# Kernel tuning notes

Hardware: AMD Instinct MI355X
Metric: run time of the kernel (lower is better)

## Reference

```python
import jax, jax.numpy as jnp
import numpy as np


def setup_inputs() -> dict:
    key = jax.random.key(0)
    inputs = jax.random.normal(key, (8, 4096, 512), dtype=jnp.float32)
    return {"inputs": inputs}


def reference(inputs) -> jnp.ndarray:
    # Faithful math: out = (X @ X^T) @ X  per batch.
    # Expressed via the associativity-equivalent X @ (X^T @ X), which computes
    # the identical result while avoiding the O(S^2) intermediate (S >> D).
    gram = jnp.einsum('bsd,bse->bde', inputs, inputs)   # [B, D, D]
    out = jnp.einsum('bsd,bde->bse', inputs, gram)      # [B, S, D]
    return out
```

## Files before the change

### kernel.cpp

```cpp
#include <hip/hip_runtime.h>
#include <hip/hip_bf16.h>


typedef __attribute__((ext_vector_type(8))) short short8;
typedef __attribute__((ext_vector_type(4))) float floatx4;

#define BM 128
#define BN 128
#define BK 32

#define BATCH 8
#define SEQ 4096
#define DIM 512
#define NSPLIT_K2 4

__device__ __forceinline__ void async_copy16(const __hip_bfloat16* g, __hip_bfloat16* l) {
  __builtin_amdgcn_global_load_lds((const __attribute__((address_space(1))) void*)g,
                                   (__attribute__((address_space(3))) void*)l, 16, 0, 0);
}

__global__ __launch_bounds__(256) void transpose_cast_kernel(
    const float* __restrict__ X, __hip_bfloat16* __restrict__ Xt) {
  __shared__ float tile[64][65];
  const int b = blockIdx.z;
  const int s0 = blockIdx.x * 64;
  const int d0 = blockIdx.y * 64;
  const int tid = threadIdx.x;
  const int tx = tid & 63;
  const int ty = tid >> 6;
  const float* Xb = X + (long)b * SEQ * DIM;
  __hip_bfloat16* Xtb = Xt + (long)b * DIM * SEQ;
#pragma unroll
  for (int r = 0; r < 64; r += 4)
    tile[r + ty][tx] = Xb[(long)(s0 + r + ty) * DIM + d0 + tx];
  __syncthreads();
#pragma unroll
  for (int it = 0; it < 2; ++it) {
    const int idx = it * 256 + tid;
    const int dl = idx >> 3;
    const int so = (idx & 7) * 8;
    union { short8 v; __hip_bfloat16 e[8]; } u;
#pragma unroll
    for (int j = 0; j < 8; ++j) u.e[j] = __float2bfloat16(tile[so + j][dl]);
    *(short8*)&Xtb[(long)(d0 + dl) * SEQ + s0 + so] = u.v;
  }
}

template <int NSPLIT, bool AFP32>
__global__ __launch_bounds__(256) void gemm_bt_kernel(
    const float* __restrict__ Af, const __hip_bfloat16* __restrict__ Ab,
    const __hip_bfloat16* __restrict__ Bt, float* __restrict__ C,
    int K, int lda, int ldb, int ldc, long strideA, long strideB, long strideC) {
  __shared__ __align__(16) __hip_bfloat16 As[BM * BK];
  __shared__ __align__(16) __hip_bfloat16 Bs[BN * BK];

  const int bz = blockIdx.z;
  const int b = bz / NSPLIT;
  const int split = bz % NSPLIT;
  const int klen = K / NSPLIT;
  const int kb = split * klen;

  const int m0 = blockIdx.y * BM;
  const int n0 = blockIdx.x * BN;
  const int tid = threadIdx.x;
  const int w = tid >> 6;
  const int lane = tid & 63;
  const int r16 = lane & 15;
  const int kg = lane >> 4;
  const int wr = w >> 1;
  const int wc = w & 1;

  const float* Afb = AFP32 ? Af + b * strideA : nullptr;
  const __hip_bfloat16* Abb = AFP32 ? nullptr : Ab + b * strideA;
  const __hip_bfloat16* Btb = Bt + b * strideB;
  float* Cb = C + (long)bz * strideC;

  const floatx4 vzero = {0.f, 0.f, 0.f, 0.f};
  floatx4 acc[4][4];
#pragma unroll
  for (int i = 0; i < 4; ++i)
#pragma unroll
    for (int j = 0; j < 4; ++j) acc[i][j] = vzero;

  for (int k0 = kb; k0 < kb + klen; k0 += BK) {
#pragma unroll
    for (int q = 0; q < 2; ++q) {
      const __hip_bfloat16* gb =
          Btb + (long)(n0 + w * 32 + q * 16 + (lane >> 2)) * ldb + k0 + (lane & 3) * 8;
      async_copy16(gb, &Bs[(w * 32 + q * 16) * BK]);
    }
    if constexpr (!AFP32) {
#pragma unroll
      for (int q = 0; q < 2; ++q) {
        const __hip_bfloat16* ga =
            Abb + (long)(m0 + w * 32 + q * 16 + (lane >> 2)) * lda + k0 + (lane & 3) * 8;
        async_copy16(ga, &As[(w * 32 + q * 16) * BK]);
      }
    } else {
      const int row = tid >> 1;
      const int half = tid & 1;
      const float* ar = Afb + (long)(m0 + row) * lda + k0 + half * 16;
      float f[16];
      *(float4*)(f + 0)  = *(const float4*)(ar + 0);
      *(float4*)(f + 4)  = *(const float4*)(ar + 4);
      *(float4*)(f + 8)  = *(const float4*)(ar + 8);
      *(float4*)(f + 12) = *(const float4*)(ar + 12);
      union { short8 v[2]; __hip_bfloat16 e[16]; } u;
#pragma unroll
      for (int t = 0; t < 16; ++t) u.e[t] = __float2bfloat16(f[t]);
      short8* dst = (short8*)&As[row * BK + half * 16];
      dst[0] = u.v[0];
      dst[1] = u.v[1];
    }
    __syncthreads();

    short8 a[4], bfrag[4];
#pragma unroll
    for (int i = 0; i < 4; ++i)
      a[i] = *(const short8*)&As[(wr * 64 + i * 16 + r16) * BK + kg * 8];
#pragma unroll
    for (int j = 0; j < 4; ++j)
      bfrag[j] = *(const short8*)&Bs[(wc * 64 + j * 16 + r16) * BK + kg * 8];
#pragma unroll
    for (int i = 0; i < 4; ++i)
#pragma unroll
      for (int j = 0; j < 4; ++j)
        acc[i][j] = __builtin_amdgcn_mfma_f32_16x16x32_bf16(a[i], bfrag[j], acc[i][j], 0, 0, 0);
    __syncthreads();
  }

#pragma unroll
  for (int i = 0; i < 4; ++i) {
    const int row_base = m0 + wr * 64 + i * 16 + kg * 4;
#pragma unroll
    for (int j = 0; j < 4; ++j) {
      const int col = n0 + wc * 64 + j * 16 + r16;
#pragma unroll
      for (int r = 0; r < 4; ++r)
        Cb[(long)(row_base + r) * ldc + col] = acc[i][j][r];
    }
  }
}

__global__ __launch_bounds__(256) void reduce_cast_kernel(
    const float* __restrict__ P, __hip_bfloat16* __restrict__ G) {
  const int DD4 = DIM * DIM / 4;
  const long idx = (long)blockIdx.x * 256 + threadIdx.x;
  const int b = (int)(idx / DD4);
  const int e = (int)(idx % DD4);
  const float4* base = (const float4*)P + (long)(b * NSPLIT_K2) * DD4 + e;
  float4 s0 = base[0];
  float4 s1 = base[DD4];
  float4 s2 = base[2 * DD4];
  float4 s3 = base[3 * DD4];
  float4 s;
  s.x = (s0.x + s1.x) + (s2.x + s3.x);
  s.y = (s0.y + s1.y) + (s2.y + s3.y);
  s.z = (s0.z + s1.z) + (s2.z + s3.z);
  s.w = (s0.w + s1.w) + (s2.w + s3.w);
  union { short s4[4]; uint2 v; } u;
  u.s4[0] = __bfloat16_as_short(__float2bfloat16(s.x));
  u.s4[1] = __bfloat16_as_short(__float2bfloat16(s.y));
  u.s4[2] = __bfloat16_as_short(__float2bfloat16(s.z));
  u.s4[3] = __bfloat16_as_short(__float2bfloat16(s.w));
  *(uint2*)&G[idx * 4] = u.v;
}

extern "C" void kernel_launch(void* const* d_in, const int* in_sizes, int n_in,
                              void* d_out, int out_size, void* d_ws, size_t ws_size,
                              hipStream_t stream) {
  const float* X = (const float*)d_in[0];
  float* out = (float*)d_out;
  __hip_bfloat16* Xt = (__hip_bfloat16*)d_out;
  float* partials = (float*)((char*)d_out + (long)BATCH * DIM * SEQ * 2);
  __hip_bfloat16* gram = (__hip_bfloat16*)d_ws;

  transpose_cast_kernel<<<dim3(SEQ / 64, DIM / 64, BATCH), 256, 0, stream>>>(X, Xt);

  gemm_bt_kernel<NSPLIT_K2, false>
      <<<dim3(DIM / BN, DIM / BM, BATCH * NSPLIT_K2), 256, 0, stream>>>(
          nullptr, Xt, Xt, partials, SEQ, SEQ, SEQ, DIM,
          (long)DIM * SEQ, (long)DIM * SEQ, (long)DIM * DIM);

  reduce_cast_kernel<<<dim3(BATCH * DIM * DIM / 4 / 256), 256, 0, stream>>>(
      partials, gram);

  gemm_bt_kernel<1, true>
      <<<dim3(DIM / BN, SEQ / BM, BATCH), 256, 0, stream>>>(
          X, nullptr, gram, out, DIM, DIM, DIM, DIM,
          (long)SEQ * DIM, (long)DIM * DIM, (long)SEQ * DIM);
}
```

Before: 197.6 us.

## Emit bf16 copy of X in transpose pass; swizzle and prefetch second GEMM

The transpose kernel now also writes a row-major bf16 copy of X into workspace, so the second GEMM can load A with async global-to-LDS copies instead of reading fp32 and converting every tile. The second GEMM's block index is remapped so consecutive blocks spread across the eight XCDs, aiming for better L2 reuse of the gram matrix. For the fp32 fallback path, the next A tile is register-prefetched before the MFMA work. This adds an extra bf16 write of X and depends on having enough workspace.

Result: faster. 187.1 us (-5.3%).

```diff
diff --git a/kernel.cpp b/kernel.cpp
--- a/kernel.cpp
+++ b/kernel.cpp
@@ -20,7 +20,8 @@
 }
 
 __global__ __launch_bounds__(256) void transpose_cast_kernel(
-    const float* __restrict__ X, __hip_bfloat16* __restrict__ Xt) {
+    const float* __restrict__ X, __hip_bfloat16* __restrict__ Xt,
+    __hip_bfloat16* __restrict__ Xb16) {
   __shared__ float tile[64][65];
   const int b = blockIdx.z;
   const int s0 = blockIdx.x * 64;
@@ -44,9 +45,22 @@
     for (int j = 0; j < 8; ++j) u.e[j] = __float2bfloat16(tile[so + j][dl]);
     *(short8*)&Xtb[(long)(d0 + dl) * SEQ + s0 + so] = u.v;
   }
-}
-
-template <int NSPLIT, bool AFP32>
+  if (Xb16 != nullptr) {
+    __hip_bfloat16* Xcb = Xb16 + (long)b * SEQ * DIM;
+#pragma unroll
+    for (int it = 0; it < 2; ++it) {
+      const int idx = it * 256 + tid;
+      const int sl = idx >> 3;
+      const int dc = idx & 7;
+      union { short8 v; __hip_bfloat16 e[8]; } u;
+#pragma unroll
+      for (int j = 0; j < 8; ++j) u.e[j] = __float2bfloat16(tile[sl][dc * 8 + j]);
+      *(short8*)&Xcb[(long)(s0 + sl) * DIM + d0 + dc * 8] = u.v;
+    }
+  }
+}
+
+template <int NSPLIT, bool AFP32, bool SWZ>
 __global__ __launch_bounds__(256) void gemm_bt_kernel(
     const float* __restrict__ Af, const __hip_bfloat16* __restrict__ Ab,
     const __hip_bfloat16* __restrict__ Bt, float* __restrict__ C,
@@ -54,14 +68,24 @@
   __shared__ __align__(16) __hip_bfloat16 As[BM * BK];
   __shared__ __align__(16) __hip_bfloat16 Bs[BN * BK];
 
-  const int bz = blockIdx.z;
+  int bz, m0, n0;
+  if constexpr (SWZ) {
+    const int lin = blockIdx.x;
+    bz = blockIdx.z;
+    const int xcd = lin & 7;
+    const int t = lin >> 3;
+    n0 = (t & 3) * BN;
+    m0 = ((t >> 2) * 8 + xcd) * BM;
+  } else {
+    bz = blockIdx.z;
+    m0 = blockIdx.y * BM;
+    n0 = blockIdx.x * BN;
+  }
   const int b = bz / NSPLIT;
   const int split = bz % NSPLIT;
   const int klen = K / NSPLIT;
   const int kb = split * klen;
 
-  const int m0 = blockIdx.y * BM;
-  const int n0 = blockIdx.x * BN;
   const int tid = threadIdx.x;
   const int w = tid >> 6;
   const int lane = tid & 63;
@@ -82,6 +106,17 @@
 #pragma unroll
     for (int j = 0; j < 4; ++j) acc[i][j] = vzero;
 
+  const int arow = tid >> 1;
+  const int ahalf = tid & 1;
+  float f[16];
+  if constexpr (AFP32) {
+    const float* ar = Afb + (long)(m0 + arow) * lda + kb + ahalf * 16;
+    *(float4*)(f + 0)  = *(const float4*)(ar + 0);
+    *(float4*)(f + 4)  = *(const float4*)(ar + 4);
+    *(float4*)(f + 8)  = *(const float4*)(ar + 8);
+    *(float4*)(f + 12) = *(const float4*)(ar + 12);
+  }
+
   for (int k0 = kb; k0 < kb + klen; k0 += BK) {
 #pragma unroll
     for (int q = 0; q < 2; ++q) {
@@ -97,22 +132,24 @@
         async_copy16(ga, &As[(w * 32 + q * 16) * BK]);
       }
     } else {
-      const int row = tid >> 1;
-      const int half = tid & 1;
-      const float* ar = Afb + (long)(m0 + row) * lda + k0 + half * 16;
-      float f[16];
-      *(float4*)(f + 0)  = *(const float4*)(ar + 0);
-      *(float4*)(f + 4)  = *(const float4*)(ar + 4);
-      *(float4*)(f + 8)  = *(const float4*)(ar + 8);
-      *(float4*)(f + 12) = *(const float4*)(ar + 12);
       union { short8 v[2]; __hip_bfloat16 e[16]; } u;
 #pragma unroll
       for (int t = 0; t < 16; ++t) u.e[t] = __float2bfloat16(f[t]);
-      short8* dst = (short8*)&As[row * BK + half * 16];
+      short8* dst = (short8*)&As[arow * BK + ahalf * 16];
       dst[0] = u.v[0];
       dst[1] = u.v[1];
     }
     __syncthreads();
+
+    if constexpr (AFP32) {
+      if (k0 + BK < kb + klen) {
+        const float* ar = Afb + (long)(m0 + arow) * lda + (k0 + BK) + ahalf * 16;
+        *(float4*)(f + 0)  = *(const float4*)(ar + 0);
+        *(float4*)(f + 4)  = *(const float4*)(ar + 4);
+        *(float4*)(f + 8)  = *(const float4*)(ar + 8);
+        *(float4*)(f + 12) = *(const float4*)(ar + 12);
+      }
+    }
 
     short8 a[4], bfrag[4];
 #pragma unroll
@@ -171,13 +208,17 @@
                               hipStream_t stream) {
   const float* X = (const float*)d_in[0];
   float* out = (float*)d_out;
+  const long xtBytes = (long)BATCH * DIM * SEQ * 2;
+  const long gramBytes = (long)BATCH * DIM * DIM * 2;
   __hip_bfloat16* Xt = (__hip_bfloat16*)d_out;
-  float* partials = (float*)((char*)d_out + (long)BATCH * DIM * SEQ * 2);
+  float* partials = (float*)((char*)d_out + xtBytes);
   __hip_bfloat16* gram = (__hip_bfloat16*)d_ws;
-
-  transpose_cast_kernel<<<dim3(SEQ / 64, DIM / 64, BATCH), 256, 0, stream>>>(X, Xt);
-
-  gemm_bt_kernel<NSPLIT_K2, false>
+  const bool fast = ws_size >= (size_t)(gramBytes + xtBytes);
+  __hip_bfloat16* Xb16 = fast ? (__hip_bfloat16*)((char*)d_ws + gramBytes) : nullptr;
+
+  transpose_cast_kernel<<<dim3(SEQ / 64, DIM / 64, BATCH), 256, 0, stream>>>(X, Xt, Xb16);
+
+  gemm_bt_kernel<NSPLIT_K2, false, false>
       <<<dim3(DIM / BN, DIM / BM, BATCH * NSPLIT_K2), 256, 0, stream>>>(
           nullptr, Xt, Xt, partials, SEQ, SEQ, SEQ, DIM,
           (long)DIM * SEQ, (long)DIM * SEQ, (long)DIM * DIM);
@@ -185,8 +226,13 @@
   reduce_cast_kernel<<<dim3(BATCH * DIM * DIM / 4 / 256), 256, 0, stream>>>(
       partials, gram);
 
-  gemm_bt_kernel<1, true>
-      <<<dim3(DIM / BN, SEQ / BM, BATCH), 256, 0, stream>>>(
-          X, nullptr, gram, out, DIM, DIM, DIM, DIM,
-          (long)SEQ * DIM, (long)DIM * DIM, (long)SEQ * DIM);
-}
+  if (fast) {
+    gemm_bt_kernel<1, false, true><<<dim3(128, 1, BATCH), 256, 0, stream>>>(
+        nullptr, Xb16, gram, out, DIM, DIM, DIM, DIM,
+        (long)SEQ * DIM, (long)DIM * DIM, (long)SEQ * DIM);
+  } else {
+    gemm_bt_kernel<1, true, true><<<dim3(128, 1, BATCH), 256, 0, stream>>>(
+        X, nullptr, gram, out, DIM, DIM, DIM, DIM,
+        (long)SEQ * DIM, (long)DIM * DIM, (long)SEQ * DIM);
+  }
+}
```
